# Kernel tuning notes

Hardware: AMD Instinct MI355X
Metric: run time of the kernel (lower is better)

## Reference

```python
import jax, jax.numpy as jnp
import numpy as np


def _construct_cayley(metric):
    """Build the dense geometric-product (Cayley) table for a diagonal metric,
    with blades in short-lex order (sorted by grade, then bitmap value).
    cayley[i, j, k] = sign s.t. out_j = sum_{i,k} a_i * cayley[i,j,k] * b_k.
    """
    d = len(metric)
    n = 1 << d  # n_blades = 2**dim
    bitmaps = sorted(range(n), key=lambda bm: (bin(bm).count("1"), bm))
    bitmap_to_index = {bm: i for i, bm in enumerate(bitmaps)}
    cayley = np.zeros((n, n, n), dtype=np.float32)
    for ia, abm in enumerate(bitmaps):
        for ib, bbm in enumerate(bitmaps):
            # canonical reordering sign: count basis-vector swaps
            t = abm >> 1
            swaps = 0
            while t:
                swaps += bin(t & bbm).count("1")
                t >>= 1
            sign = -1.0 if (swaps & 1) else 1.0
            # metric contribution from annihilated (shared) basis vectors
            meet = abm & bbm
            for i in range(d):
                if meet & (1 << i):
                    sign *= metric[i]
            out_bm = abm ^ bbm
            cayley[ia, bitmap_to_index[out_bm], ib] = sign
    return cayley


METRIC = [1, 1, 1]
BATCH, CHANNELS = 65536, 64
N_BLADES = 1 << len(METRIC)  # 8


def setup_inputs() -> dict:
    key = jax.random.key(0)
    ka, kb = jax.random.split(key)
    a = jax.random.normal(ka, (BATCH, CHANNELS, N_BLADES), dtype=jnp.float32)
    b = jax.random.normal(kb, (BATCH, CHANNELS, N_BLADES), dtype=jnp.float32)
    cayley = jnp.asarray(_construct_cayley(METRIC))  # [8, 8, 8] buffer
    return {"a": a, "b": b, "cayley": cayley}


def reference(a, b, cayley):
    # CliffordAlgebra.geometric_product: torch.einsum('...i,ijk,...k->...j', a, cayley, b)
    return jnp.einsum("...i,ijk,...k->...j", a, cayley, b)
```

## Files before the change

### kernel.cpp

```cpp
#include <hip/hip_runtime.h>


typedef float v4f __attribute__((ext_vector_type(4)));

__global__ __launch_bounds__(256) void clifford_gp_kernel(
    const v4f* __restrict__ a4, const v4f* __restrict__ b4,
    v4f* __restrict__ o4, int n_mv)
{
    int t = blockIdx.x * blockDim.x + threadIdx.x;
    if (t >= n_mv) return;

    v4f alo = a4[2 * t], ahi = a4[2 * t + 1];
    v4f blo = b4[2 * t], bhi = b4[2 * t + 1];

    float a0 = alo.x, a1 = alo.y, a2 = alo.z, a3 = alo.w;
    float A4 = ahi.x, a5 = ahi.y, a6 = ahi.z, a7 = ahi.w;
    float b0 = blo.x, b1 = blo.y, b2 = blo.z, b3 = blo.w;
    float B4 = bhi.x, b5 = bhi.y, b6 = bhi.z, b7 = bhi.w;

    v4f olo, ohi;
    olo.x = a0*b0 + a1*b1 + a2*b2 + a3*b3 - A4*B4 - a5*b5 - a6*b6 - a7*b7;
    olo.y = a0*b1 + a1*b0 - a2*B4 + A4*b2 - a3*b5 + a5*b3 - a6*b7 - a7*b6;
    olo.z = a0*b2 + a2*b0 + a1*B4 - A4*b1 - a3*b6 + a6*b3 + a5*b7 + a7*b5;
    olo.w = a0*b3 + a3*b0 + a1*b5 - a5*b1 + a2*b6 - a6*b2 - A4*b7 - a7*B4;
    ohi.x = a0*B4 + A4*b0 + a1*b2 - a2*b1 + a3*b7 + a7*b3 - a5*b6 + a6*b5;
    ohi.y = a0*b5 + a5*b0 + a1*b3 - a3*b1 - a2*b7 - a7*b2 + A4*b6 - a6*B4;
    ohi.z = a0*b6 + a6*b0 + a2*b3 - a3*b2 + a1*b7 + a7*b1 - A4*b5 + a5*B4;
    ohi.w = a0*b7 + a7*b0 + a1*b6 + a6*b1 - a2*b5 - a5*b2 + a3*B4 + A4*b3;

    __builtin_nontemporal_store(olo, &o4[2 * t]);
    __builtin_nontemporal_store(ohi, &o4[2 * t + 1]);
}

extern "C" void kernel_launch(void* const* d_in, const int* in_sizes, int n_in,
                              void* d_out, int out_size, void* d_ws, size_t ws_size,
                              hipStream_t stream) {
    const v4f* a = (const v4f*)d_in[0];
    const v4f* b = (const v4f*)d_in[1];
    v4f* out = (v4f*)d_out;
    int n_mv = in_sizes[0] / 8;
    int block = 256;
    int grid = (n_mv + block - 1) / block;
    clifford_gp_kernel<<<grid, block, 0, stream>>>(a, b, out, n_mv);
}
```

Measured before the change: 75.26 us.

## Split each multivector across two lanes with shuffle exchange for coalesced loads

```diff
diff --git a/kernel.cpp b/kernel.cpp
--- a/kernel.cpp
+++ b/kernel.cpp
@@ -5,18 +5,29 @@
 
 __global__ __launch_bounds__(256) void clifford_gp_kernel(
     const v4f* __restrict__ a4, const v4f* __restrict__ b4,
-    v4f* __restrict__ o4, int n_mv)
+    v4f* __restrict__ o4, int n_chunks)
 {
     int t = blockIdx.x * blockDim.x + threadIdx.x;
-    if (t >= n_mv) return;
+    if (t >= n_chunks) return;
 
-    v4f alo = a4[2 * t], ahi = a4[2 * t + 1];
-    v4f blo = b4[2 * t], bhi = b4[2 * t + 1];
+    v4f ma = a4[t];
+    v4f mb = b4[t];
 
-    float a0 = alo.x, a1 = alo.y, a2 = alo.z, a3 = alo.w;
-    float A4 = ahi.x, a5 = ahi.y, a6 = ahi.z, a7 = ahi.w;
-    float b0 = blo.x, b1 = blo.y, b2 = blo.z, b3 = blo.w;
-    float B4 = bhi.x, b5 = bhi.y, b6 = bhi.z, b7 = bhi.w;
+    v4f oa, ob;
+    oa.x = __shfl_xor(ma.x, 1); oa.y = __shfl_xor(ma.y, 1);
+    oa.z = __shfl_xor(ma.z, 1); oa.w = __shfl_xor(ma.w, 1);
+    ob.x = __shfl_xor(mb.x, 1); ob.y = __shfl_xor(mb.y, 1);
+    ob.z = __shfl_xor(mb.z, 1); ob.w = __shfl_xor(mb.w, 1);
+
+    bool lo = (t & 1) == 0;
+    float a0 = lo ? ma.x : oa.x, a1 = lo ? ma.y : oa.y;
+    float a2 = lo ? ma.z : oa.z, a3 = lo ? ma.w : oa.w;
+    float A4 = lo ? oa.x : ma.x, a5 = lo ? oa.y : ma.y;
+    float a6 = lo ? oa.z : ma.z, a7 = lo ? oa.w : ma.w;
+    float b0 = lo ? mb.x : ob.x, b1 = lo ? mb.y : ob.y;
+    float b2 = lo ? mb.z : ob.z, b3 = lo ? mb.w : ob.w;
+    float B4 = lo ? ob.x : mb.x, b5 = lo ? ob.y : mb.y;
+    float b6 = lo ? ob.z : mb.z, b7 = lo ? ob.w : mb.w;
 
     v4f olo, ohi;
     olo.x = a0*b0 + a1*b1 + a2*b2 + a3*b3 - A4*B4 - a5*b5 - a6*b6 - a7*b7;
@@ -28,8 +39,12 @@
     ohi.z = a0*b6 + a6*b0 + a2*b3 - a3*b2 + a1*b7 + a7*b1 - A4*b5 + a5*B4;
     ohi.w = a0*b7 + a7*b0 + a1*b6 + a6*b1 - a2*b5 - a5*b2 + a3*B4 + A4*b3;
 
-    __builtin_nontemporal_store(olo, &o4[2 * t]);
-    __builtin_nontemporal_store(ohi, &o4[2 * t + 1]);
+    v4f r;
+    r.x = lo ? olo.x : ohi.x;
+    r.y = lo ? olo.y : ohi.y;
+    r.z = lo ? olo.z : ohi.z;
+    r.w = lo ? olo.w : ohi.w;
+    o4[t] = r;
 }
 
 extern "C" void kernel_launch(void* const* d_in, const int* in_sizes, int n_in,
@@ -38,8 +53,8 @@
     const v4f* a = (const v4f*)d_in[0];
     const v4f* b = (const v4f*)d_in[1];
     v4f* out = (v4f*)d_out;
-    int n_mv = in_sizes[0] / 8;
+    int n_chunks = in_sizes[0] / 4;
     int block = 256;
-    int grid = (n_mv + block - 1) / block;
-    clifford_gp_kernel<<<grid, block, 0, stream>>>(a, b, out, n_mv);
+    int grid = (n_chunks + block - 1) / block;
+    clifford_gp_kernel<<<grid, block, 0, stream>>>(a, b, out, n_chunks);
 }
```

After: 72.91 us. 1.03x faster.
